# Kernel tuning notes

Measured on AMD Instinct MI355X. Metric: run time of the kernel, lower is better.

## Reference

```python
import jax, jax.numpy as jnp
import numpy as np

B, S, E, P = 4, 2048, 1024, 4096

def setup_inputs() -> dict:
    key = jax.random.key(0)
    kx, kk, kv = jax.random.split(key, 3)
    x = jax.random.normal(kx, (B, S, E), dtype=jnp.float32)
    K = jax.random.normal(kk, (P, E), dtype=jnp.float32)
    V = jax.random.normal(kv, (P, E), dtype=jnp.float32)
    return {"x": x, "K": K, "V": V}

def reference(x, K, V):
    # scores: [B, S, P] = x @ K^T scaled by 1/sqrt(E)
    scale = jnp.asarray(x.shape[-1], x.dtype) ** -0.5
    scores = jnp.einsum('bse,pe->bsp', x, K) * scale
    attn = jax.nn.softmax(scores, axis=-1)
    # output: [B, S, E] = attn @ V
    return jnp.einsum('bsp,pe->bse', attn, V)
```

## Files before the change

kernel.cpp:

```cpp
#include <hip/hip_runtime.h>
#include <hip/hip_bf16.h>

typedef __attribute__((ext_vector_type(8))) short bf16x8;
typedef __attribute__((ext_vector_type(4))) float f32x4;
typedef __attribute__((ext_vector_type(8))) unsigned short u16x8;
typedef __attribute__((ext_vector_type(2))) unsigned short u16x2;

__device__ __forceinline__ unsigned short f2bf(float f) {
  union { float f; unsigned u; } c; c.f = f;
  unsigned u = c.u;
  u = (u + 0x7FFFu + ((u >> 16) & 1u)) >> 16;
  return (unsigned short)u;
}

__device__ __forceinline__ void gld_lds16(const void* g, void* l) {
  __builtin_amdgcn_global_load_lds(
      (__attribute__((address_space(1))) unsigned int*)g,
      (__attribute__((address_space(3))) unsigned int*)l,
      16, 0, 0);
}

#define BAR() asm volatile("s_barrier" ::: "memory")

__global__ void cvt_all(const float* __restrict__ x, unsigned short* __restrict__ x16,
                        const float* __restrict__ Kw, unsigned short* __restrict__ K16,
                        const float* __restrict__ V, unsigned short* __restrict__ Vt) {
  const int b = blockIdx.x;
  const int tid = threadIdx.x;

  if (b < 6144) {
    const float* in;
    unsigned short* out;
    int i;
    if (b < 4096) {
      in = x; out = x16; i = (b * 256 + tid) * 8;
    } else {
      in = Kw; out = K16; i = ((b - 4096) * 256 + tid) * 8;
    }
    const float4* p = (const float4*)(in + i);
    float4 a = p[0], bb = p[1];
    u16x8 r;
    r[0] = f2bf(a.x); r[1] = f2bf(a.y); r[2] = f2bf(a.z); r[3] = f2bf(a.w);
    r[4] = f2bf(bb.x); r[5] = f2bf(bb.y); r[6] = f2bf(bb.z); r[7] = f2bf(bb.w);
    *(u16x8*)(out + i) = r;
  } else {
    __shared__ unsigned short t[64][66];
    const int tile = b - 6144;
    const int p0 = (tile & 63) * 64;
    const int e0 = (tile >> 6) * 64;
    const int cg = (tid & 15) * 4;
    const int pr = tid >> 4;
#pragma unroll
    for (int i = 0; i < 4; ++i) {
      int p = pr + i * 16;
      float4 v = *(const float4*)(V + (size_t)(p0 + p) * 1024 + e0 + cg);
      u16x2 lo, hi;
      lo[0] = f2bf(v.x); lo[1] = f2bf(v.y);
      hi[0] = f2bf(v.z); hi[1] = f2bf(v.w);
      *(u16x2*)&t[p][cg] = lo;
      *(u16x2*)&t[p][cg + 2] = hi;
    }
    __syncthreads();
    const int op = (tid & 7) * 8;
    const int oe = tid >> 3;
#pragma unroll
    for (int h = 0; h < 2; ++h) {
      int e = oe + h * 32;
      u16x8 r;
#pragma unroll
      for (int i = 0; i < 8; ++i) r[i] = t[op + i][e];
      *(u16x8*)(Vt + (size_t)(e0 + e) * 4096 + p0 + op) = r;
    }
  }
}

template <int EPI>
__global__ __launch_bounds__(512, 2) void gemm8p(
    const unsigned short* __restrict__ A, const unsigned short* __restrict__ B,
    unsigned short* __restrict__ Pout, float* __restrict__ lsum,
    float* __restrict__ Cout, const float* __restrict__ lin, float scale) {
  constexpr int BM = EPI ? 128 : 256;
  constexpr int Kd = EPI ? 4096 : 1024;
  constexpr int Nc = EPI ? 1024 : 4096;
  constexpr int NT = Kd / 64;
  constexpr int AU = BM / 128;
  constexpr int NU = AU + 2;
  constexpr int M_rep = BM / 32;
  constexpr int PH = M_rep / 2;

  __shared__ __align__(16) char lds[2 * NU * 16384];

  const int tid = threadIdx.x;
  const int lane = tid & 63;
  const int w = tid >> 6;
  const int wm = w >> 2;
  const int wn = w & 3;
  const int q = lane >> 4;
  const int ml = lane & 15;

  const int bid = blockIdx.x;
  const int wg = (bid & 7) * (EPI ? 32 : 64) + (bid >> 3);
  const int m_t = EPI ? (wg >> 2) : (wg >> 4);
  const int n_t = EPI ? (wg & 3) : (wg & 15);
  const int row0 = m_t * BM;
  const int col0 = n_t * 256;

  const int cr = tid >> 3;
  const int ss = (tid & 7) ^ (cr & 7);
  char* ldsw = lds + w * 1024;

  const int ccB = (q ^ (ml & 7)) * 16;
  const int aOff = (EPI ? 0 : wm) * 16384 + ((EPI ? wm * 64 : 0) + ml) * 128 + ccB;
  const int bOff = (AU + (wn >> 1)) * 16384 + ((wn & 1) * 64 + ml) * 128 + ccB;

  f32x4 acc[M_rep][4] = {};

  auto stA = [&](int a, int t, int buf) {
    const unsigned short* s = A + (size_t)(row0 + a * 128 + cr) * Kd + t * 64 + ss * 8;
    char* d = ldsw + (buf * NU + a) * 16384;
    gld_lds16(s, d);
    gld_lds16(s + (size_t)64 * Kd, d + 8192);
  };
  auto stB = [&](int b, int t, int buf) {
    const unsigned short* s = B + (size_t)(col0 + b * 128 + cr) * Kd + t * 64 + ss * 8;
    char* d = ldsw + (buf * NU + AU + b) * 16384;
    gld_lds16(s, d);
    gld_lds16(s + (size_t)64 * Kd, d + 8192);
  };

#pragma unroll
  for (int a = 0; a < AU; ++a) stA(a, 0, 0);
  stB(0, 0, 0); stB(1, 0, 0);
  stB(0, 1, 1); stB(1, 1, 1);
  asm volatile("s_waitcnt vmcnt(4)" ::: "memory");
  BAR();

  for (int g = 0; g < NT; ++g) {
    const char* base = lds + (g & 1) * (NU * 16384);
    const int tA = (g + 1) & (NT - 1);
    const int bufA = (g + 1) & 1;
    const int tB = (g + 2) & (NT - 1);
    const int bufB = g & 1;

    bf16x8 bF[4][2];
#pragma unroll
    for (int ni = 0; ni < 4; ++ni)
#pragma unroll
      for (int ks = 0; ks < 2; ++ks)
        bF[ni][ks] = *(const bf16x8*)(base + (bOff ^ (ks * 64)) + ni * 2048);

#pragma unroll
    for (int p = 0; p < PH; ++p) {
      bf16x8 aF[2][2];
#pragma unroll
      for (int i = 0; i < 2; ++i)
#pragma unroll
        for (int ks = 0; ks < 2; ++ks)
          aF[i][ks] = *(const bf16x8*)(base + ((aOff ^ (ks * 64)) + (2 * p + i) * 2048));

      if constexpr (EPI == 0) {
        if (p == 0) stA(0, tA, bufA);
        else if (p == 1) stA(1, tA, bufA);
        else if (p == 2) stB(0, tB, bufB);
        else stB(1, tB, bufB);
      } else {
        if (p == 0) stA(0, tA, bufA);
        else { stB(0, tB, bufB); stB(1, tB, bufB); }
      }

      BAR();
      __builtin_amdgcn_s_setprio(1);
#pragma unroll
      for (int ks = 0; ks < 2; ++ks)
#pragma unroll
        for (int i = 0; i < 2; ++i)
#pragma unroll
          for (int ni = 0; ni < 4; ++ni)
            acc[2 * p + i][ni] = __builtin_amdgcn_mfma_f32_16x16x32_bf16(
                aF[i][ks], bF[ni][ks], acc[2 * p + i][ni], 0, 0, 0);
      __builtin_amdgcn_s_setprio(0);
      if (p == PH - 1) asm volatile("s_waitcnt vmcnt(4)" ::: "memory");
      BAR();
    }
  }

  if constexpr (EPI == 0) {
#pragma unroll
    for (int mi = 0; mi < M_rep; ++mi) {
#pragma unroll
      for (int j = 0; j < 4; ++j) {
        const int gr = row0 + wm * (BM / 2) + mi * 16 + q * 4 + j;
        float rsum = 0.f;
#pragma unroll
        for (int ni = 0; ni < 4; ++ni) {
          const int gc = col0 + wn * 64 + ni * 16 + ml;
          float pv = exp2f(acc[mi][ni][j] * scale);
          rsum += pv;
          Pout[(size_t)gr * Nc + gc] = f2bf(pv);
        }
        rsum += __shfl_xor(rsum, 1);
        rsum += __shfl_xor(rsum, 2);
        rsum += __shfl_xor(rsum, 4);
        rsum += __shfl_xor(rsum, 8);
        if (ml == 0) atomicAdd(&lsum[gr], rsum);
      }
    }
  } else {
#pragma unroll
    for (int mi = 0; mi < M_rep; ++mi) {
#pragma unroll
      for (int j = 0; j < 4; ++j) {
        const int gr = row0 + wm * (BM / 2) + mi * 16 + q * 4 + j;
        const float rl = 1.0f / lin[gr];
#pragma unroll
        for (int ni = 0; ni < 4; ++ni) {
          const int gc = col0 + wn * 64 + ni * 16 + ml;
          Cout[(size_t)gr * Nc + gc] = acc[mi][ni][j] * rl;
        }
      }
    }
  }
}

extern "C" void kernel_launch(void* const* d_in, const int* in_sizes, int n_in,
                              void* d_out, int out_size, void* d_ws,
                              size_t ws_size, hipStream_t stream) {
  const float* x = (const float*)d_in[0];
  const float* Kw = (const float*)d_in[1];
  const float* Vw = (const float*)d_in[2];
  float* out = (float*)d_out;
  char* ws = (char*)d_ws;

  unsigned short* x16  = (unsigned short*)(ws);
  unsigned short* K16  = (unsigned short*)(ws + (16u << 20));
  unsigned short* V16t = (unsigned short*)(ws + (24u << 20));
  float*          lsum = (float*)(ws + (32u << 20));
  unsigned short* P16  = (unsigned short*)(ws + (33u << 20));

  hipMemsetAsync(lsum, 0, 8192 * sizeof(float), stream);
  cvt_all<<<7168, 256, 0, stream>>>(x, x16, Kw, K16, Vw, V16t);

  gemm8p<0><<<512, 512, 0, stream>>>(
      x16, K16, P16, lsum, nullptr, nullptr,
      0.03125f * 1.44269504088896340736f);
  gemm8p<1><<<256, 512, 0, stream>>>(
      P16, V16t, nullptr, nullptr, out, lsum, 0.f);
}
```

Before: 260.0 us.

## Fuse x fp32-to-bf16 conversion into first GEMM's A-tile loading

The first GEMM now reads x directly as fp32 through registers, converts it to bf16 and writes the swizzled LDS tile itself, so the separate conversion pass over x and its bf16 workspace copy are gone. The conversion kernel now handles only K and V and also zeroes lsum, which replaces the memset launch. The cost is that the first GEMM reads twice as many A bytes through VGPRs, adds conversion ALU work and register pressure, and introduces extra waitcnt and barrier points inside the pipelined loop.

```diff
diff --git a/kernel.cpp b/kernel.cpp
--- a/kernel.cpp
+++ b/kernel.cpp
@@ -22,30 +22,24 @@
 
 #define BAR() asm volatile("s_barrier" ::: "memory")
 
-__global__ void cvt_all(const float* __restrict__ x, unsigned short* __restrict__ x16,
-                        const float* __restrict__ Kw, unsigned short* __restrict__ K16,
-                        const float* __restrict__ V, unsigned short* __restrict__ Vt) {
+__global__ void cvt_kv(const float* __restrict__ Kw, unsigned short* __restrict__ K16,
+                       const float* __restrict__ V, unsigned short* __restrict__ Vt,
+                       float* __restrict__ lsum) {
   const int b = blockIdx.x;
   const int tid = threadIdx.x;
-
-  if (b < 6144) {
-    const float* in;
-    unsigned short* out;
-    int i;
-    if (b < 4096) {
-      in = x; out = x16; i = (b * 256 + tid) * 8;
-    } else {
-      in = Kw; out = K16; i = ((b - 4096) * 256 + tid) * 8;
-    }
-    const float4* p = (const float4*)(in + i);
+  if (b < 32) lsum[b * 256 + tid] = 0.f;
+
+  if (b < 2048) {
+    const int i = (b * 256 + tid) * 8;
+    const float4* p = (const float4*)(Kw + i);
     float4 a = p[0], bb = p[1];
     u16x8 r;
     r[0] = f2bf(a.x); r[1] = f2bf(a.y); r[2] = f2bf(a.z); r[3] = f2bf(a.w);
     r[4] = f2bf(bb.x); r[5] = f2bf(bb.y); r[6] = f2bf(bb.z); r[7] = f2bf(bb.w);
-    *(u16x8*)(out + i) = r;
+    *(u16x8*)(K16 + i) = r;
   } else {
     __shared__ unsigned short t[64][66];
-    const int tile = b - 6144;
+    const int tile = b - 2048;
     const int p0 = (tile & 63) * 64;
     const int e0 = (tile >> 6) * 64;
     const int cg = (tid & 15) * 4;
@@ -76,7 +70,7 @@
 
 template <int EPI>
 __global__ __launch_bounds__(512, 2) void gemm8p(
-    const unsigned short* __restrict__ A, const unsigned short* __restrict__ B,
+    const void* __restrict__ Ap, const unsigned short* __restrict__ B,
     unsigned short* __restrict__ Pout, float* __restrict__ lsum,
     float* __restrict__ Cout, const float* __restrict__ lin, float scale) {
   constexpr int BM = EPI ? 128 : 256;
@@ -115,9 +109,12 @@
 
   f32x4 acc[M_rep][4] = {};
 
-  auto stA = [&](int a, int t, int buf) {
-    const unsigned short* s = A + (size_t)(row0 + a * 128 + cr) * Kd + t * 64 + ss * 8;
-    char* d = ldsw + (buf * NU + a) * 16384;
+  const unsigned short* A16 = (const unsigned short*)Ap;
+  const float* Af = (const float*)Ap;
+
+  auto stA1 = [&](int t, int buf) {
+    const unsigned short* s = A16 + (size_t)(row0 + cr) * Kd + t * 64 + ss * 8;
+    char* d = ldsw + (buf * NU) * 16384;
     gld_lds16(s, d);
     gld_lds16(s + (size_t)64 * Kd, d + 8192);
   };
@@ -128,12 +125,51 @@
     gld_lds16(s + (size_t)64 * Kd, d + 8192);
   };
 
-#pragma unroll
-  for (int a = 0; a < AU; ++a) stA(a, 0, 0);
-  stB(0, 0, 0); stB(1, 0, 0);
-  stB(0, 1, 1); stB(1, 1, 1);
-  asm volatile("s_waitcnt vmcnt(4)" ::: "memory");
-  BAR();
+  const float* pAx[4];
+  if constexpr (EPI == 0) {
+#pragma unroll
+    for (int u = 0; u < 2; ++u)
+#pragma unroll
+      for (int j = 0; j < 2; ++j)
+        pAx[u * 2 + j] = Af + (size_t)(row0 + u * 128 + j * 64 + cr) * 1024 + ss * 8;
+  }
+  float4 aR[8];
+  auto ldAx = [&](int t) {
+#pragma unroll
+    for (int k = 0; k < 4; ++k) {
+      aR[2 * k] = *(const float4*)(pAx[k] + t * 64);
+      aR[2 * k + 1] = *(const float4*)(pAx[k] + t * 64 + 4);
+    }
+  };
+  auto wrAx = [&](int buf) {
+#pragma unroll
+    for (int k = 0; k < 4; ++k) {
+      const int u = k >> 1, j = k & 1;
+      u16x8 c;
+      c[0] = f2bf(aR[2 * k].x); c[1] = f2bf(aR[2 * k].y);
+      c[2] = f2bf(aR[2 * k].z); c[3] = f2bf(aR[2 * k].w);
+      c[4] = f2bf(aR[2 * k + 1].x); c[5] = f2bf(aR[2 * k + 1].y);
+      c[6] = f2bf(aR[2 * k + 1].z); c[7] = f2bf(aR[2 * k + 1].w);
+      const int r = j * 64 + cr;
+      *(u16x8*)(lds + (buf * NU + u) * 16384 + (r * 8 + (tid & 7)) * 16) = c;
+    }
+  };
+
+  if constexpr (EPI == 0) {
+    ldAx(0);
+    stB(0, 0, 0); stB(1, 0, 0);
+    stB(0, 1, 1); stB(1, 1, 1);
+    asm volatile("s_waitcnt vmcnt(8)" ::: "memory");
+    wrAx(0);
+    asm volatile("s_waitcnt vmcnt(4) lgkmcnt(0)" ::: "memory");
+    BAR();
+  } else {
+    stA1(0, 0);
+    stB(0, 0, 0); stB(1, 0, 0);
+    stB(0, 1, 1); stB(1, 1, 1);
+    asm volatile("s_waitcnt vmcnt(4)" ::: "memory");
+    BAR();
+  }
 
   for (int g = 0; g < NT; ++g) {
     const char* base = lds + (g & 1) * (NU * 16384);
@@ -159,12 +195,11 @@
           aF[i][ks] = *(const bf16x8*)(base + ((aOff ^ (ks * 64)) + (2 * p + i) * 2048));
 
       if constexpr (EPI == 0) {
-        if (p == 0) stA(0, tA, bufA);
-        else if (p == 1) stA(1, tA, bufA);
-        else if (p == 2) stB(0, tB, bufB);
-        else stB(1, tB, bufB);
+        if (p == 0) ldAx(tA);
+        else if (p == 1) stB(0, tB, bufB);
+        else if (p == 2) stB(1, tB, bufB);
       } else {
-        if (p == 0) stA(0, tA, bufA);
+        if (p == 0) stA1(tA, bufA);
         else { stB(0, tB, bufB); stB(1, tB, bufB); }
       }
 
@@ -179,7 +214,16 @@
             acc[2 * p + i][ni] = __builtin_amdgcn_mfma_f32_16x16x32_bf16(
                 aF[i][ks], bF[ni][ks], acc[2 * p + i][ni], 0, 0, 0);
       __builtin_amdgcn_s_setprio(0);
-      if (p == PH - 1) asm volatile("s_waitcnt vmcnt(4)" ::: "memory");
+      if (p == PH - 1) {
+        if constexpr (EPI == 0) {
+          asm volatile("s_waitcnt vmcnt(4)" ::: "memory");
+          __builtin_amdgcn_sched_barrier(0);
+          wrAx(bufA);
+          asm volatile("s_waitcnt lgkmcnt(0)" ::: "memory");
+        } else {
+          asm volatile("s_waitcnt vmcnt(4)" ::: "memory");
+        }
+      }
       BAR();
     }
   }
@@ -231,17 +275,15 @@
   float* out = (float*)d_out;
   char* ws = (char*)d_ws;
 
-  unsigned short* x16  = (unsigned short*)(ws);
   unsigned short* K16  = (unsigned short*)(ws + (16u << 20));
   unsigned short* V16t = (unsigned short*)(ws + (24u << 20));
   float*          lsum = (float*)(ws + (32u << 20));
   unsigned short* P16  = (unsigned short*)(ws + (33u << 20));
 
-  hipMemsetAsync(lsum, 0, 8192 * sizeof(float), stream);
-  cvt_all<<<7168, 256, 0, stream>>>(x, x16, Kw, K16, Vw, V16t);
+  cvt_kv<<<3072, 256, 0, stream>>>(Kw, K16, Vw, V16t, lsum);
 
   gemm8p<0><<<512, 512, 0, stream>>>(
-      x16, K16, P16, lsum, nullptr, nullptr,
+      x, K16, P16, lsum, nullptr, nullptr,
       0.03125f * 1.44269504088896340736f);
   gemm8p<1><<<256, 512, 0, stream>>>(
       P16, V16t, nullptr, nullptr, out, lsum, 0.f);
```

Measured after the change: 311.5 us. 19.8% more time.

## Load A operand directly to registers in first GEMM and fold memset into convert

Applied to the files above, without the earlier changes.

The first GEMM (x·Kᵀ) now reads its A tile straight from global memory into registers, double-buffered across iterations, and keeps only B staged through LDS. This halves its LDS footprint and drops the A LDS round trip and one barrier per phase. The lsum zeroing moves into the convert kernel, removing a separate memset launch. The cost is higher register pressure and uncoalesced per-lane A loads, which may hurt occupancy or memory efficiency.

```diff
diff --git a/kernel.cpp b/kernel.cpp
--- a/kernel.cpp
+++ b/kernel.cpp
@@ -24,9 +24,11 @@
 
 __global__ void cvt_all(const float* __restrict__ x, unsigned short* __restrict__ x16,
                         const float* __restrict__ Kw, unsigned short* __restrict__ K16,
-                        const float* __restrict__ V, unsigned short* __restrict__ Vt) {
+                        const float* __restrict__ V, unsigned short* __restrict__ Vt,
+                        float* __restrict__ lsum) {
   const int b = blockIdx.x;
   const int tid = threadIdx.x;
+  if (b < 32) lsum[b * 256 + tid] = 0.f;
 
   if (b < 6144) {
     const float* in;
@@ -74,21 +76,12 @@
   }
 }
 
-template <int EPI>
-__global__ __launch_bounds__(512, 2) void gemm8p(
+__global__ __launch_bounds__(512, 2) void gemm_flat(
     const unsigned short* __restrict__ A, const unsigned short* __restrict__ B,
-    unsigned short* __restrict__ Pout, float* __restrict__ lsum,
-    float* __restrict__ Cout, const float* __restrict__ lin, float scale) {
-  constexpr int BM = EPI ? 128 : 256;
-  constexpr int Kd = EPI ? 4096 : 1024;
-  constexpr int Nc = EPI ? 1024 : 4096;
-  constexpr int NT = Kd / 64;
-  constexpr int AU = BM / 128;
-  constexpr int NU = AU + 2;
-  constexpr int M_rep = BM / 32;
-  constexpr int PH = M_rep / 2;
-
-  __shared__ __align__(16) char lds[2 * NU * 16384];
+    unsigned short* __restrict__ Pout, float* __restrict__ lsum, float scale) {
+  constexpr int NT = 16;
+
+  __shared__ __align__(16) char lds[65536];
 
   const int tid = threadIdx.x;
   const int lane = tid & 63;
@@ -99,25 +92,173 @@
   const int ml = lane & 15;
 
   const int bid = blockIdx.x;
-  const int wg = (bid & 7) * (EPI ? 32 : 64) + (bid >> 3);
-  const int m_t = EPI ? (wg >> 2) : (wg >> 4);
-  const int n_t = EPI ? (wg & 3) : (wg & 15);
-  const int row0 = m_t * BM;
-  const int col0 = n_t * 256;
+  const int wg = (bid & 7) * 64 + (bid >> 3);
+  const int row0 = (wg >> 4) * 256;
+  const int col0 = (wg & 15) * 256;
 
   const int cr = tid >> 3;
   const int ss = (tid & 7) ^ (cr & 7);
   char* ldsw = lds + w * 1024;
+  auto stB = [&](int b, int t, int buf) {
+    const unsigned short* s = B + (size_t)(col0 + b * 128 + cr) * 1024 + t * 64 + ss * 8;
+    char* d = ldsw + (buf * 2 + b) * 16384;
+    gld_lds16(s, d);
+    gld_lds16(s + (size_t)64 * 1024, d + 8192);
+  };
 
   const int ccB = (q ^ (ml & 7)) * 16;
-  const int aOff = (EPI ? 0 : wm) * 16384 + ((EPI ? wm * 64 : 0) + ml) * 128 + ccB;
+  const int bOff = (wn >> 1) * 16384 + ((wn & 1) * 64 + ml) * 128 + ccB;
+
+  const unsigned short* aB = A + (size_t)(row0 + wm * 128 + ml) * 1024 + q * 8;
+  auto ldA = [&](int t, bf16x8 (&dst)[2][2][2], int half) {
+    const unsigned short* s = aB + (size_t)half * 4 * 16 * 1024 + t * 64;
+#pragma unroll
+    for (int pp = 0; pp < 2; ++pp)
+#pragma unroll
+      for (int i = 0; i < 2; ++i)
+#pragma unroll
+        for (int ks = 0; ks < 2; ++ks)
+          dst[pp][i][ks] =
+              *(const bf16x8*)(s + (size_t)(pp * 2 + i) * 16 * 1024 + ks * 32);
+  };
+
+  f32x4 acc[8][4] = {};
+
+  bf16x8 AA1[2][2][2], AA2[2][2][2], BB1[2][2][2], BB2[2][2][2];
+
+  ldA(0, AA1, 0);
+  stB(0, 0, 0); stB(1, 0, 0);
+  ldA(0, AA2, 1);
+  stB(0, 1, 1); stB(1, 1, 1);
+  asm volatile("s_waitcnt vmcnt(12)" ::: "memory");
+  BAR();
+
+  auto tile = [&](int g, bf16x8 (&aC1)[2][2][2], bf16x8 (&aC2)[2][2][2],
+                  bf16x8 (&aN1)[2][2][2], bf16x8 (&aN2)[2][2][2]) {
+    const char* base = lds + (g & 1) * 32768;
+    const int tA = (g + 1) & (NT - 1);
+    const int tB = (g + 2) & (NT - 1);
+
+    bf16x8 bF[4][2];
+#pragma unroll
+    for (int ni = 0; ni < 4; ++ni)
+#pragma unroll
+      for (int ks = 0; ks < 2; ++ks)
+        bF[ni][ks] = *(const bf16x8*)(base + (bOff ^ (ks * 64)) + ni * 2048);
+
+    ldA(tA, aN1, 0);
+
+    __builtin_amdgcn_s_setprio(1);
+#pragma unroll
+    for (int ks = 0; ks < 2; ++ks)
+#pragma unroll
+      for (int i = 0; i < 2; ++i)
+#pragma unroll
+        for (int ni = 0; ni < 4; ++ni)
+          acc[i][ni] = __builtin_amdgcn_mfma_f32_16x16x32_bf16(
+              aC1[0][i][ks], bF[ni][ks], acc[i][ni], 0, 0, 0);
+    __builtin_amdgcn_s_setprio(0);
+    BAR();
+
+    stB(0, tB, g & 1);
+    stB(1, tB, g & 1);
+    __builtin_amdgcn_s_setprio(1);
+#pragma unroll
+    for (int ks = 0; ks < 2; ++ks)
+#pragma unroll
+      for (int i = 0; i < 2; ++i)
+#pragma unroll
+        for (int ni = 0; ni < 4; ++ni)
+          acc[2 + i][ni] = __builtin_amdgcn_mfma_f32_16x16x32_bf16(
+              aC1[1][i][ks], bF[ni][ks], acc[2 + i][ni], 0, 0, 0);
+    __builtin_amdgcn_s_setprio(0);
+
+    ldA(tA, aN2, 1);
+    __builtin_amdgcn_s_setprio(1);
+#pragma unroll
+    for (int ks = 0; ks < 2; ++ks)
+#pragma unroll
+      for (int i = 0; i < 2; ++i)
+#pragma unroll
+        for (int ni = 0; ni < 4; ++ni)
+          acc[4 + i][ni] = __builtin_amdgcn_mfma_f32_16x16x32_bf16(
+              aC2[0][i][ks], bF[ni][ks], acc[4 + i][ni], 0, 0, 0);
+
+#pragma unroll
+    for (int ks = 0; ks < 2; ++ks)
+#pragma unroll
+      for (int i = 0; i < 2; ++i)
+#pragma unroll
+        for (int ni = 0; ni < 4; ++ni)
+          acc[6 + i][ni] = __builtin_amdgcn_mfma_f32_16x16x32_bf16(
+              aC2[1][i][ks], bF[ni][ks], acc[6 + i][ni], 0, 0, 0);
+    __builtin_amdgcn_s_setprio(0);
+
+    asm volatile("s_waitcnt vmcnt(12)" ::: "memory");
+    BAR();
+  };
+
+  for (int gg = 0; gg < NT; gg += 2) {
+    tile(gg, AA1, AA2, BB1, BB2);
+    tile(gg + 1, BB1, BB2, AA1, AA2);
+  }
+
+#pragma unroll
+  for (int mi = 0; mi < 8; ++mi) {
+#pragma unroll
+    for (int j = 0; j < 4; ++j) {
+      const int gr = row0 + wm * 128 + mi * 16 + q * 4 + j;
+      float rsum = 0.f;
+#pragma unroll
+      for (int ni = 0; ni < 4; ++ni) {
+        const int gc = col0 + wn * 64 + ni * 16 + ml;
+        float pv = exp2f(acc[mi][ni][j] * scale);
+        rsum += pv;
+        Pout[(size_t)gr * 4096 + gc] = f2bf(pv);
+      }
+      rsum += __shfl_xor(rsum, 1);
+      rsum += __shfl_xor(rsum, 2);
+      rsum += __shfl_xor(rsum, 4);
+      rsum += __shfl_xor(rsum, 8);
+      if (ml == 0) atomicAdd(&lsum[gr], rsum);
+    }
+  }
+}
+
+__global__ __launch_bounds__(512, 2) void gemm2(
+    const unsigned short* __restrict__ A, const unsigned short* __restrict__ B,
+    float* __restrict__ Cout, const float* __restrict__ lin) {
+  constexpr int BM = 128, Kd = 4096, Nc = 1024, NT = 64;
+  constexpr int AU = 1, NU = 3, M_rep = 4, PH = 2;
+
+  __shared__ __align__(16) char lds[2 * NU * 16384];
+
+  const int tid = threadIdx.x;
+  const int lane = tid & 63;
+  const int w = tid >> 6;
+  const int wm = w >> 2;
+  const int wn = w & 3;
+  const int q = lane >> 4;
+  const int ml = lane & 15;
+
+  const int bid = blockIdx.x;
+  const int wg = (bid & 7) * 32 + (bid >> 3);
+  const int row0 = (wg >> 2) * BM;
+  const int col0 = (wg & 3) * 256;
+
+  const int cr = tid >> 3;
+  const int ss = (tid & 7) ^ (cr & 7);
+  char* ldsw = lds + w * 1024;
+
+  const int ccB = (q ^ (ml & 7)) * 16;
+  const int aOff = (wm * 64 + ml) * 128 + ccB;
   const int bOff = (AU + (wn >> 1)) * 16384 + ((wn & 1) * 64 + ml) * 128 + ccB;
 
   f32x4 acc[M_rep][4] = {};
 
-  auto stA = [&](int a, int t, int buf) {
-    const unsigned short* s = A + (size_t)(row0 + a * 128 + cr) * Kd + t * 64 + ss * 8;
-    char* d = ldsw + (buf * NU + a) * 16384;
+  auto stA = [&](int t, int buf) {
+    const unsigned short* s = A + (size_t)(row0 + cr) * Kd + t * 64 + ss * 8;
+    char* d = ldsw + (buf * NU) * 16384;
     gld_lds16(s, d);
     gld_lds16(s + (size_t)64 * Kd, d + 8192);
   };
@@ -128,8 +269,7 @@
     gld_lds16(s + (size_t)64 * Kd, d + 8192);
   };
 
-#pragma unroll
-  for (int a = 0; a < AU; ++a) stA(a, 0, 0);
+  stA(0, 0);
   stB(0, 0, 0); stB(1, 0, 0);
   stB(0, 1, 1); stB(1, 1, 1);
   asm volatile("s_waitcnt vmcnt(4)" ::: "memory");
@@ -158,15 +298,8 @@
         for (int ks = 0; ks < 2; ++ks)
           aF[i][ks] = *(const bf16x8*)(base + ((aOff ^ (ks * 64)) + (2 * p + i) * 2048));
 
-      if constexpr (EPI == 0) {
-        if (p == 0) stA(0, tA, bufA);
-        else if (p == 1) stA(1, tA, bufA);
-        else if (p == 2) stB(0, tB, bufB);
-        else stB(1, tB, bufB);
-      } else {
-        if (p == 0) stA(0, tA, bufA);
-        else { stB(0, tB, bufB); stB(1, tB, bufB); }
-      }
+      if (p == 0) stA(tA, bufA);
+      else { stB(0, tB, bufB); stB(1, tB, bufB); }
 
       BAR();
       __builtin_amdgcn_s_setprio(1);
@@ -184,39 +317,16 @@
     }
   }
 
-  if constexpr (EPI == 0) {
-#pragma unroll
-    for (int mi = 0; mi < M_rep; ++mi) {
-#pragma unroll
-      for (int j = 0; j < 4; ++j) {
-        const int gr = row0 + wm * (BM / 2) + mi * 16 + q * 4 + j;
-        float rsum = 0.f;
-#pragma unroll
-        for (int ni = 0; ni < 4; ++ni) {
-          const int gc = col0 + wn * 64 + ni * 16 + ml;
-          float pv = exp2f(acc[mi][ni][j] * scale);
-          rsum += pv;
-          Pout[(size_t)gr * Nc + gc] = f2bf(pv);
-        }
-        rsum += __shfl_xor(rsum, 1);
-        rsum += __shfl_xor(rsum, 2);
-        rsum += __shfl_xor(rsum, 4);
-        rsum += __shfl_xor(rsum, 8);
-        if (ml == 0) atomicAdd(&lsum[gr], rsum);
-      }
-    }
-  } else {
-#pragma unroll
-    for (int mi = 0; mi < M_rep; ++mi) {
-#pragma unroll
-      for (int j = 0; j < 4; ++j) {
-        const int gr = row0 + wm * (BM / 2) + mi * 16 + q * 4 + j;
-        const float rl = 1.0f / lin[gr];
-#pragma unroll
-        for (int ni = 0; ni < 4; ++ni) {
-          const int gc = col0 + wn * 64 + ni * 16 + ml;
-          Cout[(size_t)gr * Nc + gc] = acc[mi][ni][j] * rl;
-        }
+#pragma unroll
+  for (int mi = 0; mi < M_rep; ++mi) {
+#pragma unroll
+    for (int j = 0; j < 4; ++j) {
+      const int gr = row0 + wm * (BM / 2) + mi * 16 + q * 4 + j;
+      const float rl = 1.0f / lin[gr];
+#pragma unroll
+      for (int ni = 0; ni < 4; ++ni) {
+        const int gc = col0 + wn * 64 + ni * 16 + ml;
+        Cout[(size_t)gr * Nc + gc] = acc[mi][ni][j] * rl;
       }
     }
   }
@@ -237,12 +347,9 @@
   float*          lsum = (float*)(ws + (32u << 20));
   unsigned short* P16  = (unsigned short*)(ws + (33u << 20));
 
-  hipMemsetAsync(lsum, 0, 8192 * sizeof(float), stream);
-  cvt_all<<<7168, 256, 0, stream>>>(x, x16, Kw, K16, Vw, V16t);
-
-  gemm8p<0><<<512, 512, 0, stream>>>(
-      x16, K16, P16, lsum, nullptr, nullptr,
-      0.03125f * 1.44269504088896340736f);
-  gemm8p<1><<<256, 512, 0, stream>>>(
-      P16, V16t, nullptr, nullptr, out, lsum, 0.f);
-}
+  cvt_all<<<7168, 256, 0, stream>>>(x, x16, Kw, K16, Vw, V16t, lsum);
+
+  gemm_flat<<<512, 512, 0, stream>>>(
+      x16, K16, P16, lsum, 0.03125f * 1.44269504088896340736f);
+  gemm2<<<256, 512, 0, stream>>>(P16, V16t, out, lsum);
+}
```

Measured after the change: 443.7 us. 70.6% more time.
